# Optimization experiments

Measured on AMD Instinct MI355X. Metric: run time of the kernel, lower is better.

## Reference

```python
import jax, jax.numpy as jnp
import numpy as np

B, NSEQ, SEQ_PER = 2, 4, 256
S = NSEQ * SEQ_PER            # total sequence (stocks interleaved along seq dim)
D, H, HD = 1024, 16, 64       # d_model, nhead, head_dim
HD2, HD4 = HD // 2, HD // 4
DFF = 4096
LAMBDA_INIT = 0.2             # lambda_init_fn(0) = 0.8 - 0.6*exp(0)
SCALING = 1.0 / float(np.sqrt(HD2))
EPS_DEF = float(np.finfo(np.float32).eps)   # torch RMSNorm default eps (eps=None)
EPS_ATTN = 1e-5


def _rms(x, w, eps):
    return x * jax.lax.rsqrt(jnp.mean(x * x, axis=-1, keepdims=True) + eps) * w


def _rope(x, fc):
    # x: (B, T, NSEQ, 2H, HD2); fc: (T, HD4, 2) holding (cos, sin)
    xr = x.reshape(x.shape[:-1] + (HD4, 2))
    c = fc[None, :, None, None, :, 0]
    s = fc[None, :, None, None, :, 1]
    x0, x1 = xr[..., 0], xr[..., 1]
    return jnp.stack([x0 * c - x1 * s, x0 * s + x1 * c], axis=-1).reshape(x.shape)


def setup_inputs():
    key = jax.random.key(0)
    ks = jax.random.split(key, 16)
    def w(i, shape, std=0.02):
        return jax.random.normal(ks[i], shape, jnp.float32) * std
    # true RoPE table for seq_per_stock-1 positions
    t = jnp.arange(SEQ_PER - 1, dtype=jnp.float32)[:, None]
    inv = 1.0 / (10000.0 ** (jnp.arange(HD4, dtype=jnp.float32) / HD4))
    ang = t * inv[None, :]
    return {
        "x": jax.random.normal(ks[0], (B, S, D), jnp.float32),
        "freqs_cis": jnp.stack([jnp.cos(ang), jnp.sin(ang)], axis=-1),
        "w_norm1": jnp.ones((D,), jnp.float32),
        "w_norm2": jnp.ones((D,), jnp.float32),
        "Wq": w(1, (H * HD, D)), "bq": jnp.zeros((H * HD,), jnp.float32),
        "Wk": w(2, (H * HD, D)), "bk": jnp.zeros((H * HD,), jnp.float32),
        "Wv": w(3, (H * HD, D)), "bv": jnp.zeros((H * HD,), jnp.float32),
        "Wo": w(4, (D, H * HD)), "bo": jnp.zeros((D,), jnp.float32),
        "lq1": w(5, (HD2,), 0.1), "lk1": w(6, (HD2,), 0.1),
        "lq2": w(7, (HD2,), 0.1), "lk2": w(8, (HD2,), 0.1),
        "w_attn_norm": jnp.ones((HD,), jnp.float32),
        "Wg": w(9, (2 * DFF, D)), "bg": jnp.zeros((2 * DFF,), jnp.float32),
        "Wout": w(10, (D, DFF)), "bout": jnp.zeros((D,), jnp.float32),
    }


def reference(x, freqs_cis, w_norm1, w_norm2, Wq, bq, Wk, bk, Wv, bv, Wo, bo,
              lq1, lk1, lq2, lk2, w_attn_norm, Wg, bg, Wout, bout):
    Bz, Sz, _ = x.shape
    h = _rms(x, w_norm1, EPS_DEF)
    q = (h @ Wq.T + bq).reshape(Bz, SEQ_PER, NSEQ, 2 * H, HD2)
    k = (h @ Wk.T + bk).reshape(Bz, SEQ_PER, NSEQ, 2 * H, HD2)
    v = (h @ Wv.T + bv).reshape(Bz, Sz, H, HD).transpose(0, 2, 1, 3)   # (B,H,S,HD), interleaved order
    # RoPE on all but the first per-stock timestep; same freqs for every stock
    q = jnp.concatenate([q[:, :1], _rope(q[:, 1:], freqs_cis)], axis=1)
    k = jnp.concatenate([k[:, :1], _rope(k[:, 1:], freqs_cis)], axis=1)
    # reorder q/k to stock-major flat sequence (torch permute(0,4,1,2,3)+reshape)
    q = q.transpose(0, 2, 1, 3, 4).reshape(Bz, Sz, 2 * H, HD2).transpose(0, 2, 1, 3)
    k = k.transpose(0, 2, 1, 3, 4).reshape(Bz, Sz, 2 * H, HD2).transpose(0, 2, 1, 3)
    scores = jnp.einsum('bhqd,bhkd->bhqk', q, k) * SCALING              # (B,2H,S,S)
    causal = jnp.triu(jnp.ones((SEQ_PER, SEQ_PER), bool), 1)
    mask = jnp.tile(causal, (NSEQ, NSEQ))   # block-tiled causal, as torch .repeat
    att = jnp.sign(scores) * jax.nn.softmax(
        jnp.where(mask, -1e30, jnp.abs(scores)), axis=-1)
    lam = jnp.exp(jnp.sum(lk1 * lq1)) - jnp.exp(jnp.sum(lk2 * lq2)) + LAMBDA_INIT
    att = att.reshape(Bz, H, 2, Sz, Sz)
    a1, a2 = att[:, :, 0], att[:, :, 1]
    G = jnp.mean(a1, axis=-2, keepdims=True)          # mean over queries, broadcast back
    a = jnp.where(mask, 0.0, a1 - lam * a2 + lam * G)
    ao = jnp.einsum('bhqk,bhkd->bhqd', a, v)          # v kept in interleaved order (faithful to source)
    ao = _rms(ao, w_attn_norm, EPS_ATTN)
    ao = ao.reshape(Bz, Sz, H * HD)  # flat reinterpret (B,H,S,HD)->(B,S,H*HD), matches torch reshape chain
    x = x + ao @ Wo.T + bo
    h2 = _rms(x, w_norm2, EPS_DEF)
    u, vg = jnp.split(h2 @ Wg.T + bg, 2, axis=-1)
    return x + (u * jax.nn.silu(vg)) @ Wout.T + bout
```

## Files before the change

### kernel.cpp

```cpp
#include <hip/hip_runtime.h>

#define LAMBDA_INIT 0.2f
#define SCALING 0.17677669529663687f
#define EPS_DEF 1.1920928955078125e-07f
#define EPS_ATTN 1e-5f

typedef unsigned short us4 __attribute__((ext_vector_type(4)));
typedef unsigned short us8v __attribute__((ext_vector_type(8)));
typedef float f32x4 __attribute__((ext_vector_type(4)));
typedef float f32x2 __attribute__((ext_vector_type(2)));
typedef __bf16 bf16x8 __attribute__((ext_vector_type(8)));

#define MFMA16(a, b, c) __builtin_amdgcn_mfma_f32_16x16x32_bf16((a), (b), (c), 0, 0, 0)

__device__ __forceinline__ float bf2f(unsigned short u) {
    unsigned int x = ((unsigned int)u) << 16;
    return __builtin_bit_cast(float, x);
}
__device__ __forceinline__ unsigned short f2bf(float f) {
    unsigned int x = __builtin_bit_cast(unsigned int, f);
    x += 0x7fffu + ((x >> 16) & 1u);
    return (unsigned short)(x >> 16);
}
__device__ __forceinline__ void split8(f32x4 a, f32x4 b, us8v& hi, us8v& lo) {
#pragma unroll
    for (int u = 0; u < 4; u++) {
        unsigned short h = f2bf(a[u]);
        hi[u] = h; lo[u] = f2bf(a[u] - bf2f(h));
        unsigned short h2 = f2bf(b[u]);
        hi[4 + u] = h2; lo[4 + u] = f2bf(b[u] - bf2f(h2));
    }
}
__device__ __forceinline__ bf16x8 ldb(const unsigned short* p) {
    return __builtin_bit_cast(bf16x8, *(const us8v*)p);
}

__device__ __forceinline__ float wave_sum(float v) {
#pragma unroll
    for (int o = 32; o > 0; o >>= 1) v += __shfl_down(v, o);
    return v;
}
__device__ __forceinline__ float block_sum(float v, float* red4) {
    int wv = threadIdx.x >> 6;
    float w = wave_sum(v);
    __syncthreads();
    if ((threadIdx.x & 63) == 0) red4[wv] = w;
    __syncthreads();
    return red4[0] + red4[1] + red4[2] + red4[3];
}

__global__ __launch_bounds__(256) void prep(float* __restrict__ G, float* __restrict__ lamp,
                                            const float* lq1, const float* lk1,
                                            const float* lq2, const float* lk2) {
    int i = (blockIdx.x * 256 + threadIdx.x) * 4;
    G[i] = 0.f; G[i + 1] = 0.f; G[i + 2] = 0.f; G[i + 3] = 0.f;
    if (blockIdx.x == 0 && threadIdx.x == 0) {
        float a = 0.f, c = 0.f;
        for (int d = 0; d < 32; d++) {
            a += lq1[d] * lk1[d];
            c += lq2[d] * lk2[d];
        }
        *lamp = expf(a) - expf(c) + LAMBDA_INIT;
    }
}

__global__ __launch_bounds__(256) void cvt_bf16(const float* __restrict__ s,
                                                unsigned short* __restrict__ d, int n4) {
    int i = blockIdx.x * 256 + threadIdx.x;
    if (i >= n4) return;
    f32x4 v = ((const f32x4*)s)[i];
    us4 o;
#pragma unroll
    for (int u = 0; u < 4; u++) o[u] = f2bf(v[u]);
    ((us4*)d)[i] = o;
}

template <int OUTBF>
__global__ __launch_bounds__(256) void rms_kernel(const float* __restrict__ x,
                                                  const float* __restrict__ w,
                                                  void* __restrict__ out, float eps) {
    int row = blockIdx.x;
    int tid = threadIdx.x;
    size_t base = (size_t)row * 1024 + tid * 4;
    f32x4 v = *(const f32x4*)(x + base);
    float ss = v[0]*v[0] + v[1]*v[1] + v[2]*v[2] + v[3]*v[3];
    __shared__ float red4[4];
    float tot = block_sum(ss, red4);
    float r = rsqrtf(tot * (1.0f / 1024.f) + eps);
    f32x4 wv = *(const f32x4*)(w + tid * 4);
    if (OUTBF) {
        us4 o;
#pragma unroll
        for (int i = 0; i < 4; i++) o[i] = f2bf(v[i] * r * wv[i]);
        *(us4*)((unsigned short*)out + base) = o;
    } else {
        f32x4 o;
#pragma unroll
        for (int i = 0; i < 4; i++) o[i] = v[i] * r * wv[i];
        *(f32x4*)((float*)out + base) = o;
    }
}

__global__ __launch_bounds__(256) void gemm_qkv_split(const float* __restrict__ A,
        const float* __restrict__ Wq, const float* __restrict__ Wk, const float* __restrict__ Wv,
        const float* __restrict__ bq, const float* __restrict__ bk, const float* __restrict__ bv,
        float* __restrict__ Yq, float* __restrict__ Yk, float* __restrict__ Yv) {
    const int z = blockIdx.z;
    const float* Bt  = (z == 0) ? Wq : (z == 1) ? Wk : Wv;
    const float* bias= (z == 0) ? bq : (z == 1) ? bk : bv;
    float* out       = (z == 0) ? Yq : (z == 1) ? Yk : Yv;
    const int K = 1024, N = 1024;
    __shared__ __align__(16) unsigned short Ah[64][40];
    __shared__ __align__(16) unsigned short Al[64][40];
    __shared__ __align__(16) unsigned short Bh[64][40];
    __shared__ __align__(16) unsigned short Bl[64][40];
    const int t = threadIdx.x;
    const int bm = blockIdx.x, bn = blockIdx.y;
    const int lane = t & 63, w = t >> 6;
    const int wr = w >> 1, wc = w & 1;
    const int l15 = lane & 15, lg = lane >> 4;
    const int sr = t >> 2, sc = (t & 3) * 8;

    const float* Ag = A + (size_t)(bm * 64 + sr) * K + sc;
    const float* Bg = Bt + (size_t)(bn * 64 + sr) * K + sc;

    f32x4 acc[2][2] = {};

    for (int k0 = 0; k0 < K; k0 += 32) {
        us8v ah, al, bh, bl;
        split8(*(const f32x4*)(Ag + k0), *(const f32x4*)(Ag + k0 + 4), ah, al);
        split8(*(const f32x4*)(Bg + k0), *(const f32x4*)(Bg + k0 + 4), bh, bl);
        __syncthreads();
        *(us8v*)&Ah[sr][sc] = ah;
        *(us8v*)&Al[sr][sc] = al;
        *(us8v*)&Bh[sr][sc] = bh;
        *(us8v*)&Bl[sr][sc] = bl;
        __syncthreads();
        bf16x8 afh[2], afl[2], bfh[2], bfl[2];
#pragma unroll
        for (int mi = 0; mi < 2; mi++) {
            afh[mi] = ldb(&Ah[wr * 32 + mi * 16 + l15][lg * 8]);
            afl[mi] = ldb(&Al[wr * 32 + mi * 16 + l15][lg * 8]);
        }
#pragma unroll
        for (int ni = 0; ni < 2; ni++) {
            bfh[ni] = ldb(&Bh[wc * 32 + ni * 16 + l15][lg * 8]);
            bfl[ni] = ldb(&Bl[wc * 32 + ni * 16 + l15][lg * 8]);
        }
#pragma unroll
        for (int mi = 0; mi < 2; mi++)
#pragma unroll
            for (int ni = 0; ni < 2; ni++) {
                acc[mi][ni] = MFMA16(afl[mi], bfh[ni], acc[mi][ni]);
                acc[mi][ni] = MFMA16(afh[mi], bfl[ni], acc[mi][ni]);
                acc[mi][ni] = MFMA16(afh[mi], bfh[ni], acc[mi][ni]);
            }
    }

    const int rbase = bm * 64 + wr * 32 + (lg << 2);
    const int cbase = bn * 64 + wc * 32 + l15;
#pragma unroll
    for (int mi = 0; mi < 2; mi++) {
#pragma unroll
        for (int ni = 0; ni < 2; ni++) {
            int col = cbase + ni * 16;
            float bb = bias[col];
#pragma unroll
            for (int r = 0; r < 4; r++) {
                int row = rbase + mi * 16 + r;
                out[(size_t)row * N + col] = acc[mi][ni][r] + bb;
            }
        }
    }
}

__global__ __launch_bounds__(256) void gemm_mfma_wb(const unsigned short* __restrict__ A,
                                                    const unsigned short* __restrict__ Bt,
                                                    const float* __restrict__ bias,
                                                    const float* __restrict__ res,
                                                    float* __restrict__ out,
                                                    int M, int N, int K) {
    __shared__ __align__(16) unsigned short As[64][72];
    __shared__ __align__(16) unsigned short Bs[64][72];
    const int t = threadIdx.x;
    const int bm = blockIdx.x, bn = blockIdx.y;
    const int lane = t & 63, w = t >> 6;
    const int wr = w >> 1, wc = w & 1;
    const int l15 = lane & 15, lg = lane >> 4;
    const int sr = t >> 2, sc = (t & 3) * 16;

    const unsigned short* Ag = A + (size_t)(bm * 64 + sr) * K + sc;
    const unsigned short* Bg = Bt + (size_t)(bn * 64 + sr) * K + sc;

    f32x4 acc[2][2] = {};

    for (int k0 = 0; k0 < K; k0 += 64) {
        us8v a0 = *(const us8v*)(Ag + k0);
        us8v a1 = *(const us8v*)(Ag + k0 + 8);
        us8v b0 = *(const us8v*)(Bg + k0);
        us8v b1 = *(const us8v*)(Bg + k0 + 8);
        __syncthreads();
        *(us8v*)&As[sr][sc]     = a0;
        *(us8v*)&As[sr][sc + 8] = a1;
        *(us8v*)&Bs[sr][sc]     = b0;
        *(us8v*)&Bs[sr][sc + 8] = b1;
        __syncthreads();
#pragma unroll
        for (int kk = 0; kk < 2; kk++) {
            bf16x8 af[2], bf[2];
#pragma unroll
            for (int mi = 0; mi < 2; mi++)
                af[mi] = ldb(&As[wr * 32 + mi * 16 + l15][kk * 32 + lg * 8]);
#pragma unroll
            for (int ni = 0; ni < 2; ni++)
                bf[ni] = ldb(&Bs[wc * 32 + ni * 16 + l15][kk * 32 + lg * 8]);
#pragma unroll
            for (int mi = 0; mi < 2; mi++)
#pragma unroll
                for (int ni = 0; ni < 2; ni++)
                    acc[mi][ni] = MFMA16(af[mi], bf[ni], acc[mi][ni]);
        }
    }

    const int rbase = bm * 64 + wr * 32 + (lg << 2);
    const int cbase = bn * 64 + wc * 32 + l15;
#pragma unroll
    for (int mi = 0; mi < 2; mi++) {
#pragma unroll
        for (int ni = 0; ni < 2; ni++) {
            int col = cbase + ni * 16;
            float bb = bias[col];
#pragma unroll
            for (int r = 0; r < 4; r++) {
                int row = rbase + mi * 16 + r;
                size_t oi = (size_t)row * N + col;
                out[oi] = acc[mi][ni][r] + bb + res[oi];
            }
        }
    }
}

__global__ __launch_bounds__(256) void gemm_gate_mfma(const unsigned short* __restrict__ A,
                                                      const float* __restrict__ Wg,
                                                      const float* __restrict__ bg,
                                                      unsigned short* __restrict__ mlp) {
    __shared__ __align__(16) unsigned short As[128][72];
    __shared__ __align__(16) unsigned short BsU[64][72];
    __shared__ __align__(16) unsigned short BsV[64][72];
    const int t = threadIdx.x;
    const int bm = blockIdx.x, bn = blockIdx.y;
    const int lane = t & 63, w = t >> 6;
    const int wr = w >> 1, wc = w & 1;
    const int l15 = lane & 15, lg = lane >> 4;
    const int sr = t >> 2, sc = (t & 3) * 16;

    const unsigned short* Ag  = A + (size_t)(bm * 128 + sr) * 1024 + sc;
    const unsigned short* Ag2 = Ag + (size_t)64 * 1024;
    const float* BgU = Wg + (size_t)(bn * 64 + sr) * 1024 + sc;
    const float* BgV = Wg + (size_t)(4096 + bn * 64 + sr) * 1024 + sc;

    f32x4 accU[4][2] = {};
    f32x4 accV[4][2] = {};

    for (int k0 = 0; k0 < 1024; k0 += 64) {
        us8v a0 = *(const us8v*)(Ag + k0);
        us8v a1 = *(const us8v*)(Ag + k0 + 8);
        us8v a2 = *(const us8v*)(Ag2 + k0);
        us8v a3 = *(const us8v*)(Ag2 + k0 + 8);
        f32x4 u0 = *(const f32x4*)(BgU + k0);
        f32x4 u1 = *(const f32x4*)(BgU + k0 + 4);
        f32x4 u2 = *(const f32x4*)(BgU + k0 + 8);
        f32x4 u3 = *(const f32x4*)(BgU + k0 + 12);
        f32x4 v0 = *(const f32x4*)(BgV + k0);
        f32x4 v1 = *(const f32x4*)(BgV + k0 + 4);
        f32x4 v2 = *(const f32x4*)(BgV + k0 + 8);
        f32x4 v3 = *(const f32x4*)(BgV + k0 + 12);
        us8v uw0, uw1, vw0, vw1;
#pragma unroll
        for (int u = 0; u < 4; u++) {
            uw0[u] = f2bf(u0[u]); uw0[4 + u] = f2bf(u1[u]);
            uw1[u] = f2bf(u2[u]); uw1[4 + u] = f2bf(u3[u]);
            vw0[u] = f2bf(v0[u]); vw0[4 + u] = f2bf(v1[u]);
            vw1[u] = f2bf(v2[u]); vw1[4 + u] = f2bf(v3[u]);
        }
        __syncthreads();
        *(us8v*)&As[sr][sc]          = a0;
        *(us8v*)&As[sr][sc + 8]      = a1;
        *(us8v*)&As[sr + 64][sc]     = a2;
        *(us8v*)&As[sr + 64][sc + 8] = a3;
        *(us8v*)&BsU[sr][sc]         = uw0;
        *(us8v*)&BsU[sr][sc + 8]     = uw1;
        *(us8v*)&BsV[sr][sc]         = vw0;
        *(us8v*)&BsV[sr][sc + 8]     = vw1;
        __syncthreads();
#pragma unroll
        for (int kk = 0; kk < 2; kk++) {
            bf16x8 af[4], bu[2], bv2[2];
#pragma unroll
            for (int mi = 0; mi < 4; mi++)
                af[mi] = ldb(&As[wr * 64 + mi * 16 + l15][kk * 32 + lg * 8]);
#pragma unroll
            for (int ni = 0; ni < 2; ni++) {
                bu[ni]  = ldb(&BsU[wc * 32 + ni * 16 + l15][kk * 32 + lg * 8]);
                bv2[ni] = ldb(&BsV[wc * 32 + ni * 16 + l15][kk * 32 + lg * 8]);
            }
#pragma unroll
            for (int mi = 0; mi < 4; mi++)
#pragma unroll
                for (int ni = 0; ni < 2; ni++) {
                    accU[mi][ni] = MFMA16(af[mi], bu[ni], accU[mi][ni]);
                    accV[mi][ni] = MFMA16(af[mi], bv2[ni], accV[mi][ni]);
                }
        }
    }

    const int rbase = bm * 128 + wr * 64 + (lg << 2);
    const int cbase = bn * 64 + wc * 32 + l15;
#pragma unroll
    for (int mi = 0; mi < 4; mi++) {
#pragma unroll
        for (int ni = 0; ni < 2; ni++) {
            int col = cbase + ni * 16;
            float bu_ = bg[col], bv_ = bg[4096 + col];
#pragma unroll
            for (int r = 0; r < 4; r++) {
                int row = rbase + mi * 16 + r;
                float u = accU[mi][ni][r] + bu_;
                float v = accV[mi][ni][r] + bv_;
                float s = v / (1.f + __expf(-v));
                mlp[(size_t)row * 4096 + col] = f2bf(u * s);
            }
        }
    }
}

__global__ __launch_bounds__(256) void rope_inplace(float* __restrict__ Y,
                                                    const float* __restrict__ fc) {
    int t = blockIdx.x;
    int s = t & 1023;
    int p = s >> 2;
    if (p == 0) return;
    int c0 = threadIdx.x * 4;
    float* y = Y + (size_t)t * 1024 + c0;
    int d4 = (c0 & 31) >> 1;
    f32x4 f = *(const f32x4*)(fc + ((size_t)(p - 1) * 16 + d4) * 2);
    float v0 = y[0], v1 = y[1], v2 = y[2], v3 = y[3];
    y[0] = v0 * f[0] - v1 * f[1];
    y[1] = v0 * f[1] + v1 * f[0];
    y[2] = v2 * f[2] - v3 * f[3];
    y[3] = v2 * f[3] + v3 * f[2];
}

__global__ __launch_bounds__(256) void rope_split_k(const float* __restrict__ Yk,
                                                    const float* __restrict__ fc,
                                                    unsigned short* __restrict__ KhG,
                                                    unsigned short* __restrict__ KlG) {
    int t = blockIdx.x;
    int s = t & 1023;
    int p = s >> 2;
    int c0 = threadIdx.x * 4;
    const float* y = Yk + (size_t)t * 1024 + c0;
    float v0 = y[0], v1 = y[1], v2 = y[2], v3 = y[3];
    if (p > 0) {
        int d4 = (c0 & 31) >> 1;
        f32x4 f = *(const f32x4*)(fc + ((size_t)(p - 1) * 16 + d4) * 2);
        float w0 = v0 * f[0] - v1 * f[1];
        float w1 = v0 * f[1] + v1 * f[0];
        float w2 = v2 * f[2] - v3 * f[3];
        float w3 = v2 * f[3] + v3 * f[2];
        v0 = w0; v1 = w1; v2 = w2; v3 = w3;
    }
    us4 hi, lo;
    hi[0] = f2bf(v0); lo[0] = f2bf(v0 - bf2f(hi[0]));
    hi[1] = f2bf(v1); lo[1] = f2bf(v1 - bf2f(hi[1]));
    hi[2] = f2bf(v2); lo[2] = f2bf(v2 - bf2f(hi[2]));
    hi[3] = f2bf(v3); lo[3] = f2bf(v3 - bf2f(hi[3]));
    *(us4*)(KhG + (size_t)t * 1024 + c0) = hi;
    *(us4*)(KlG + (size_t)t * 1024 + c0) = lo;
}

__global__ __launch_bounds__(256) void v_split_t(const float* __restrict__ Yv,
                                                 unsigned short* __restrict__ VtH,
                                                 unsigned short* __restrict__ VtL) {
    const int jc = blockIdx.x, h = blockIdx.y, b = blockIdx.z;
    __shared__ float tile[64][65];
    const int t = threadIdx.x;
    {
        const int jr = t >> 2, dc = (t & 3) * 16;
        const float* src = Yv + ((size_t)(b * 1024 + jc * 64 + jr) << 10) + h * 64 + dc;
        *(f32x4*)&tile[jr][dc]      = *(const f32x4*)src;
        *(f32x4*)&tile[jr][dc + 4]  = *(const f32x4*)(src + 4);
        *(f32x4*)&tile[jr][dc + 8]  = *(const f32x4*)(src + 8);
        *(f32x4*)&tile[jr][dc + 12] = *(const f32x4*)(src + 12);
    }
    __syncthreads();
    const int d = t >> 2, js = (t & 3) * 16;
    us8v h0, h1, l0, l1;
#pragma unroll
    for (int n = 0; n < 16; n++) {
        float val = tile[js + n][d];
        unsigned short hh = f2bf(val);
        unsigned short ll = f2bf(val - bf2f(hh));
        if (n < 8) { h0[n] = hh; l0[n] = ll; }
        else       { h1[n - 8] = hh; l1[n - 8] = ll; }
    }
    size_t ob = (((size_t)(b * 16 + h) * 64 + d) << 10) + jc * 64 + js;
    *(us8v*)(VtH + ob) = h0; *(us8v*)(VtH + ob + 8) = h1;
    *(us8v*)(VtL + ob) = l0; *(us8v*)(VtL + ob + 8) = l1;
}

__global__ __launch_bounds__(256) void pass_1(const float* __restrict__ Yq,
                                              const unsigned short* __restrict__ KhG,
                                              const unsigned short* __restrict__ KlG,
                                              const unsigned short* __restrict__ VtH,
                                              const unsigned short* __restrict__ VtL,
                                              const float* __restrict__ lamp,
                                              float* __restrict__ G,
                                              float* __restrict__ AOp) {
    const int blk = blockIdx.x;
    const int qc = 15 - (blk >> 5);
    const int h  = blk & 15;
    const int b  = (blk >> 4) & 1;
    const int t = threadIdx.x;
    const int lane = t & 63, w = t >> 6;
    const int l15 = lane & 15, lg = lane >> 4;

    __shared__ __align__(16) unsigned short Kh[64][72];
    __shared__ __align__(16) unsigned short Kl[64][72];
    __shared__ __align__(16) unsigned short Vth[64][72];
    __shared__ __align__(16) unsigned short Vtl[64][72];
    __shared__ __align__(16) unsigned short Wh[64][72];
    __shared__ __align__(16) unsigned short Wl[64][72];
    __shared__ float Gacc[1024];

    for (int i = t; i < 1024; i += 256) Gacc[i] = 0.f;

    us8v qh[2], ql[2];
    {
        const float* qp = Yq + ((size_t)(b * 1024 + qc * 64 + w * 16 + l15) << 10)
                          + h * 64 + lg * 8;
#pragma unroll
        for (int H = 0; H < 2; H++)
            split8(*(const f32x4*)(qp + H * 32), *(const f32x4*)(qp + H * 32 + 4), qh[H], ql[H]);
    }
    const int dq0 = w * 16 + (lg << 2);

    const int srow = t >> 2, ssub = t & 3;
    const int ptk = 4 * (srow & 15) + (srow >> 4);
    const unsigned short* KhB = KhG + ((size_t)(b * 1024) << 10) + h * 64;
    const unsigned short* KlB = KlG + ((size_t)(b * 1024) << 10) + h * 64;
    const unsigned short* VhB = VtH + (((size_t)(b * 16 + h) * 64 + srow) << 10) + ssub * 256;
    const unsigned short* VlB = VtL + (((size_t)(b * 16 + h) * 64 + srow) << 10) + ssub * 256;

    float z1r[4] = {0.f, 0.f, 0.f, 0.f};
    float z2r[4] = {0.f, 0.f, 0.f, 0.f};

    for (int kc = 0; kc <= qc; kc++) {
        __syncthreads();
        {
            const unsigned short* kh = KhB + ((size_t)(kc * 64 + ptk) << 10) + ssub * 16;
            const unsigned short* kl = KlB + ((size_t)(kc * 64 + ptk) << 10) + ssub * 16;
            *(us8v*)&Kh[srow][ssub * 16]     = *(const us8v*)kh;
            *(us8v*)&Kh[srow][ssub * 16 + 8] = *(const us8v*)(kh + 8);
            *(us8v*)&Kl[srow][ssub * 16]     = *(const us8v*)kl;
            *(us8v*)&Kl[srow][ssub * 16 + 8] = *(const us8v*)(kl + 8);
        }
        __syncthreads();
        const int kpos = kc * 16 + l15;
#pragma unroll
        for (int kf = 0; kf < 4; kf++) {
            const int krow = kf * 16 + l15;
            const int kcol = lg * 8;
            bf16x8 b1h = ldb(&Kh[krow][kcol]),      b1l = ldb(&Kl[krow][kcol]);
            bf16x8 b2h = ldb(&Kh[krow][32 + kcol]), b2l = ldb(&Kl[krow][32 + kcol]);
            f32x4 s1 = {}, s2 = {};
            s1 = MFMA16(__builtin_bit_cast(bf16x8, ql[0]), b1h, s1);
            s1 = MFMA16(__builtin_bit_cast(bf16x8, qh[0]), b1l, s1);
            s1 = MFMA16(__builtin_bit_cast(bf16x8, qh[0]), b1h, s1);
            s2 = MFMA16(__builtin_bit_cast(bf16x8, ql[1]), b2h, s2);
            s2 = MFMA16(__builtin_bit_cast(bf16x8, qh[1]), b2l, s2);
            s2 = MFMA16(__builtin_bit_cast(bf16x8, qh[1]), b2h, s2);
#pragma unroll
            for (int r = 0; r < 4; r++) {
                int pq = (qc * 64 + dq0 + r) >> 2;
                if (kpos <= pq) {
                    z1r[r] += __expf(fabsf(s1[r] * SCALING));
                    z2r[r] += __expf(fabsf(s2[r] * SCALING));
                }
            }
        }
    }
#pragma unroll
    for (int r = 0; r < 4; r++) {
        float a = z1r[r];
        a += __shfl_xor(a, 1); a += __shfl_xor(a, 2);
        a += __shfl_xor(a, 4); a += __shfl_xor(a, 8);
        z1r[r] = 1.f / fmaxf(a, 1e-20f);
        float c = z2r[r];
        c += __shfl_xor(c, 1); c += __shfl_xor(c, 2);
        c += __shfl_xor(c, 4); c += __shfl_xor(c, 8);
        z2r[r] = 1.f / fmaxf(c, 1e-20f);
    }
    const float lam = *lamp;

    f32x4 ao[4] = {};

    for (int kc = 0; kc <= qc; kc++) {
        __syncthreads();
        {
            const unsigned short* kh = KhB + ((size_t)(kc * 64 + ptk) << 10) + ssub * 16;
            const unsigned short* kl = KlB + ((size_t)(kc * 64 + ptk) << 10) + ssub * 16;
            *(us8v*)&Kh[srow][ssub * 16]     = *(const us8v*)kh;
            *(us8v*)&Kh[srow][ssub * 16 + 8] = *(const us8v*)(kh + 8);
            *(us8v*)&Kl[srow][ssub * 16]     = *(const us8v*)kl;
            *(us8v*)&Kl[srow][ssub * 16 + 8] = *(const us8v*)(kl + 8);
            const unsigned short* vh = VhB + kc * 16;
            const unsigned short* vl = VlB + kc * 16;
            *(us8v*)&Vth[srow][ssub * 16]     = *(const us8v*)vh;
            *(us8v*)&Vth[srow][ssub * 16 + 8] = *(const us8v*)(vh + 8);
            *(us8v*)&Vtl[srow][ssub * 16]     = *(const us8v*)vl;
            *(us8v*)&Vtl[srow][ssub * 16 + 8] = *(const us8v*)(vl + 8);
        }
        __syncthreads();
        const int kpos = kc * 16 + l15;
#pragma unroll
        for (int kf = 0; kf < 4; kf++) {
            const int krow = kf * 16 + l15;
            const int kcol = lg * 8;
            bf16x8 b1h = ldb(&Kh[krow][kcol]),      b1l = ldb(&Kl[krow][kcol]);
            bf16x8 b2h = ldb(&Kh[krow][32 + kcol]), b2l = ldb(&Kl[krow][32 + kcol]);
            f32x4 s1 = {}, s2 = {};
            s1 = MFMA16(__builtin_bit_cast(bf16x8, ql[0]), b1h, s1);
            s1 = MFMA16(__builtin_bit_cast(bf16x8, qh[0]), b1l, s1);
            s1 = MFMA16(__builtin_bit_cast(bf16x8, qh[0]), b1h, s1);
            s2 = MFMA16(__builtin_bit_cast(bf16x8, ql[1]), b2h, s2);
            s2 = MFMA16(__builtin_bit_cast(bf16x8, qh[1]), b2l, s2);
            s2 = MFMA16(__builtin_bit_cast(bf16x8, qh[1]), b2h, s2);
            const int kli = kf * 16 + l15;
            float colsum = 0.f;
#pragma unroll
            for (int r = 0; r < 4; r++) {
                int pq = (qc * 64 + dq0 + r) >> 2;
                float wv = 0.f, a1 = 0.f;
                if (kpos <= pq) {
                    float t1 = s1[r] * SCALING, t2 = s2[r] * SCALING;
                    float sg1 = (t1 > 0.f) ? 1.f : ((t1 < 0.f) ? -1.f : 0.f);
                    float sg2 = (t2 > 0.f) ? 1.f : ((t2 < 0.f) ? -1.f : 0.f);
                    a1 = sg1 * __expf(fabsf(t1)) * z1r[r];
                    wv = a1 - lam * (sg2 * __expf(fabsf(t2)) * z2r[r]);
                }
                colsum += a1;
                unsigned short hh = f2bf(wv);
                Wh[dq0 + r][kli] = hh;
                Wl[dq0 + r][kli] = f2bf(wv - bf2f(hh));
            }
            colsum += __shfl_xor(colsum, 16);
            colsum += __shfl_xor(colsum, 32);
            if (lane < 16) atomicAdd(&Gacc[kf * 256 + kc * 16 + lane], colsum);
        }
        __syncthreads();
#pragma unroll
        for (int kh2 = 0; kh2 < 2; kh2++) {
            bf16x8 wah = ldb(&Wh[w * 16 + l15][kh2 * 32 + lg * 8]);
            bf16x8 wal = ldb(&Wl[w * 16 + l15][kh2 * 32 + lg * 8]);
#pragma unroll
            for (int df = 0; df < 4; df++) {
                bf16x8 vbh = ldb(&Vth[df * 16 + l15][kh2 * 32 + lg * 8]);
                bf16x8 vbl = ldb(&Vtl[df * 16 + l15][kh2 * 32 + lg * 8]);
                ao[df] = MFMA16(wah, vbl, ao[df]);
                ao[df] = MFMA16(wal, vbh, ao[df]);
                ao[df] = MFMA16(wah, vbh, ao[df]);
            }
        }
    }

#pragma unroll
    for (int df = 0; df < 4; df++) {
#pragma unroll
        for (int r = 0; r < 4; r++) {
            int tq = qc * 64 + dq0 + r;
            int qrow = ((tq & 3) << 8) + (tq >> 2);
            AOp[((((size_t)(b * 16 + h)) << 10) + qrow) * 64 + df * 16 + l15] = ao[df][r];
        }
    }

    __syncthreads();
    float* Gb = G + ((size_t)(b * 16 + h) << 10);
    const int limp = (qc + 1) << 4;
    for (int idx = t; idx < 1024; idx += 256) {
        if ((idx & 255) < limp) atomicAdd(&Gb[idx], Gacc[idx]);
    }
}

__global__ __launch_bounds__(256) void pass_2a(const float* __restrict__ G,
                                               const float* __restrict__ Yv,
                                               float* __restrict__ GVpre) {
    const int h = blockIdx.x, b = blockIdx.y;
    const int t = threadIdx.x;
    __shared__ float Gl[1024];
    __shared__ float S[256][64];
    __shared__ float segsum[4][64];
    for (int i = t; i < 1024; i += 256) Gl[i] = G[((size_t)(b * 16 + h) << 10) + i];
    __syncthreads();
    const int d = t & 63, pg = t >> 6;
    const float* Yvb = Yv + ((size_t)b << 20) + h * 64 + d;
    for (int p0 = 0; p0 < 64; p0++) {
        int pos = pg * 64 + p0;
        float s = 0.f;
#pragma unroll
        for (int sq = 0; sq < 4; sq++) {
            int j = (sq << 8) + pos;
            s += Gl[j] * Yvb[(size_t)j << 10];
        }
        S[pos][d] = s;
    }
    __syncthreads();
    float acc = 0.f;
    for (int p0 = 0; p0 < 64; p0++) {
        int pos = pg * 64 + p0;
        acc += S[pos][d];
        S[pos][d] = acc;
    }
    segsum[pg][d] = acc;
    __syncthreads();
    float off = 0.f;
    for (int g = 0; g < pg; g++) off += segsum[g][d];
    float* gv = GVpre + (((size_t)(b * 16 + h)) << 14) + d;
    for (int p0 = 0; p0 < 64; p0++) {
        int pos = pg * 64 + p0;
        gv[pos << 6] = S[pos][d] + off;
    }
}

__global__ __launch_bounds__(256) void pass_2b(const float* __restrict__ AOp,
                                               const float* __restrict__ GVpre,
                                               const float* __restrict__ lamp,
                                               const float* __restrict__ wan,
                                               unsigned short* __restrict__ aoS) {
    const int qg = blockIdx.x;
    const int h = blockIdx.y, b = blockIdx.z;
    const int t = threadIdx.x;
    const int d = t & 63, rg = t >> 6;
    const float lamg = (*lamp) * (1.f / 1024.f);
    const float wv = wan[d];
    const float* aob = AOp + ((((size_t)(b * 16 + h)) << 10) + (qg << 8)) * 64 + d;
    const float* gvb = GVpre + (((size_t)(b * 16 + h)) << 14) + d;
    unsigned short* ob = aoS + ((size_t)b << 20) + ((size_t)h << 16) + ((size_t)(qg << 8) << 6) + d;
    for (int p0 = 0; p0 < 64; p0++) {
        int pq = p0 * 4 + rg;
        float ao = aob[(size_t)pq << 6] + lamg * gvb[(size_t)pq << 6];
        float ss = ao * ao;
#pragma unroll
        for (int o = 1; o < 64; o <<= 1) ss += __shfl_xor(ss, o);
        float rr_ = rsqrtf(ss * (1.f / 64.f) + EPS_ATTN);
        ob[(size_t)pq << 6] = f2bf(ao * rr_ * wv);
    }
}

extern "C" void kernel_launch(void* const* d_in, const int* in_sizes, int n_in,
                              void* d_out, int out_size, void* d_ws, size_t ws_size,
                              hipStream_t stream) {
    const float* x    = (const float*)d_in[0];
    const float* fc   = (const float*)d_in[1];
    const float* w1   = (const float*)d_in[2];
    const float* w2   = (const float*)d_in[3];
    const float* Wq   = (const float*)d_in[4];
    const float* bq   = (const float*)d_in[5];
    const float* Wk   = (const float*)d_in[6];
    const float* bk   = (const float*)d_in[7];
    const float* Wv   = (const float*)d_in[8];
    const float* bv   = (const float*)d_in[9];
    const float* Wo   = (const float*)d_in[10];
    const float* bo   = (const float*)d_in[11];
    const float* lq1  = (const float*)d_in[12];
    const float* lk1  = (const float*)d_in[13];
    const float* lq2  = (const float*)d_in[14];
    const float* lk2  = (const float*)d_in[15];
    const float* wan  = (const float*)d_in[16];
    const float* Wg   = (const float*)d_in[17];
    const float* bg   = (const float*)d_in[18];
    const float* Wout = (const float*)d_in[19];
    const float* bout = (const float*)d_in[20];

    char* ws = (char*)d_ws;
    const size_t MB = 1024 * 1024;
    float* G    = (float*)(ws);
    float* lam  = (float*)(ws + 256 * 1024);
    float* h32  = (float*)(ws + 1 * MB);
    float* Yq   = (float*)(ws + 9 * MB);
    float* Yk   = (float*)(ws + 17 * MB);
    float* Yv   = (float*)(ws + 25 * MB);
    float* AOp  = (float*)(ws + 33 * MB);
    float* GVpre= (float*)(ws + 41 * MB);
    unsigned short* WoB   = (unsigned short*)(ws + 43 * MB);
    unsigned short* WoutB = (unsigned short*)(ws + 45 * MB);
    unsigned short* KhG = (unsigned short*)(ws + 1 * MB);
    unsigned short* KlG = (unsigned short*)(ws + 5 * MB);
    unsigned short* VtH = (unsigned short*)(ws + 17 * MB);
    unsigned short* VtL = (unsigned short*)(ws + 21 * MB);
    unsigned short* aoS = (unsigned short*)(ws + 1 * MB);
    float* X1           = (float*)(ws + 9 * MB);
    unsigned short* h2b = (unsigned short*)(ws + 5 * MB);
    unsigned short* mlp = (unsigned short*)(ws + 17 * MB);

    prep<<<32, 256, 0, stream>>>(G, lam, lq1, lk1, lq2, lk2);
    cvt_bf16<<<1024, 256, 0, stream>>>(Wo, WoB, 262144);
    cvt_bf16<<<4096, 256, 0, stream>>>(Wout, WoutB, 1048576);
    rms_kernel<0><<<2048, 256, 0, stream>>>(x, w1, h32, EPS_DEF);
    gemm_qkv_split<<<dim3(32, 16, 3), 256, 0, stream>>>(h32, Wq, Wk, Wv, bq, bk, bv, Yq, Yk, Yv);
    rope_inplace<<<2048, 256, 0, stream>>>(Yq, fc);
    rope_split_k<<<2048, 256, 0, stream>>>(Yk, fc, KhG, KlG);
    v_split_t<<<dim3(16, 16, 2), 256, 0, stream>>>(Yv, VtH, VtL);
    pass_1<<<512, 256, 0, stream>>>(Yq, KhG, KlG, VtH, VtL, lam, G, AOp);
    pass_2a<<<dim3(16, 2), 256, 0, stream>>>(G, Yv, GVpre);
    pass_2b<<<dim3(4, 16, 2), 256, 0, stream>>>(AOp, GVpre, lam, wan, aoS);
    dim3 gmf(32, 16);
    gemm_mfma_wb<<<gmf, 256, 0, stream>>>(aoS, WoB, bo, x, X1, 2048, 1024, 1024);
    rms_kernel<1><<<2048, 256, 0, stream>>>(X1, w2, h2b, EPS_DEF);
    gemm_gate_mfma<<<dim3(16, 64), 256, 0, stream>>>(h2b, Wg, bg, mlp);
    gemm_mfma_wb<<<gmf, 256, 0, stream>>>(mlp, WoutB, bout, X1, (float*)d_out, 2048, 1024, 4096);
}
```

Baseline: 476.2 us.

## Pre-split QKV operands to bf16 hi/lo and pair causal query chunks per block

The QKV GEMM now reads operands that were already split into bf16 hi/lo planes by separate kernels (rms_split, cvt_split for the weights). It uses a 64-wide K step, which removes the per-tile fp32 split work and halves the number of loop iterations and barriers. pass_1 now launches 256 blocks, each handling query chunk 15-p and then chunk p, so every block does the same amount of causal work. The trade-offs are extra weight-conversion launches and traffic, bigger shared tiles, and lower grid parallelism in the attention pass.

Result: faster. 464.4 us (-2.5%).

```diff
diff --git a/kernel.cpp b/kernel.cpp
--- a/kernel.cpp
+++ b/kernel.cpp
@@ -73,6 +73,22 @@
 #pragma unroll
     for (int u = 0; u < 4; u++) o[u] = f2bf(v[u]);
     ((us4*)d)[i] = o;
+}
+
+__global__ __launch_bounds__(256) void cvt_split(const float* __restrict__ s,
+                                                 unsigned short* __restrict__ hi,
+                                                 unsigned short* __restrict__ lo, int n4) {
+    int i = blockIdx.x * 256 + threadIdx.x;
+    if (i >= n4) return;
+    f32x4 v = ((const f32x4*)s)[i];
+    us4 h, l;
+#pragma unroll
+    for (int u = 0; u < 4; u++) {
+        h[u] = f2bf(v[u]);
+        l[u] = f2bf(v[u] - bf2f(h[u]));
+    }
+    ((us4*)hi)[i] = h;
+    ((us4*)lo)[i] = l;
 }
 
 template <int OUTBF>
@@ -101,60 +117,94 @@
     }
 }
 
-__global__ __launch_bounds__(256) void gemm_qkv_split(const float* __restrict__ A,
-        const float* __restrict__ Wq, const float* __restrict__ Wk, const float* __restrict__ Wv,
+__global__ __launch_bounds__(256) void rms_split(const float* __restrict__ x,
+                                                 const float* __restrict__ w,
+                                                 unsigned short* __restrict__ hh,
+                                                 unsigned short* __restrict__ hl, float eps) {
+    int row = blockIdx.x;
+    int tid = threadIdx.x;
+    size_t base = (size_t)row * 1024 + tid * 4;
+    f32x4 v = *(const f32x4*)(x + base);
+    float ss = v[0]*v[0] + v[1]*v[1] + v[2]*v[2] + v[3]*v[3];
+    __shared__ float red4[4];
+    float tot = block_sum(ss, red4);
+    float r = rsqrtf(tot * (1.0f / 1024.f) + eps);
+    f32x4 wv = *(const f32x4*)(w + tid * 4);
+    us4 oh, ol;
+#pragma unroll
+    for (int i = 0; i < 4; i++) {
+        float val = v[i] * r * wv[i];
+        oh[i] = f2bf(val);
+        ol[i] = f2bf(val - bf2f(oh[i]));
+    }
+    *(us4*)(hh + base) = oh;
+    *(us4*)(hl + base) = ol;
+}
+
+__global__ __launch_bounds__(256) void gemm_qkv_ps(
+        const unsigned short* __restrict__ AH, const unsigned short* __restrict__ AL,
+        const unsigned short* __restrict__ WqH, const unsigned short* __restrict__ WqL,
+        const unsigned short* __restrict__ WkH, const unsigned short* __restrict__ WkL,
+        const unsigned short* __restrict__ WvH, const unsigned short* __restrict__ WvL,
         const float* __restrict__ bq, const float* __restrict__ bk, const float* __restrict__ bv,
         float* __restrict__ Yq, float* __restrict__ Yk, float* __restrict__ Yv) {
     const int z = blockIdx.z;
-    const float* Bt  = (z == 0) ? Wq : (z == 1) ? Wk : Wv;
-    const float* bias= (z == 0) ? bq : (z == 1) ? bk : bv;
-    float* out       = (z == 0) ? Yq : (z == 1) ? Yk : Yv;
+    const unsigned short* BH = (z == 0) ? WqH : (z == 1) ? WkH : WvH;
+    const unsigned short* BL = (z == 0) ? WqL : (z == 1) ? WkL : WvL;
+    const float* bias = (z == 0) ? bq : (z == 1) ? bk : bv;
+    float* out        = (z == 0) ? Yq : (z == 1) ? Yk : Yv;
     const int K = 1024, N = 1024;
-    __shared__ __align__(16) unsigned short Ah[64][40];
-    __shared__ __align__(16) unsigned short Al[64][40];
-    __shared__ __align__(16) unsigned short Bh[64][40];
-    __shared__ __align__(16) unsigned short Bl[64][40];
+    __shared__ __align__(16) unsigned short Ah[64][72];
+    __shared__ __align__(16) unsigned short Al[64][72];
+    __shared__ __align__(16) unsigned short Bh[64][72];
+    __shared__ __align__(16) unsigned short Bl[64][72];
     const int t = threadIdx.x;
     const int bm = blockIdx.x, bn = blockIdx.y;
     const int lane = t & 63, w = t >> 6;
     const int wr = w >> 1, wc = w & 1;
     const int l15 = lane & 15, lg = lane >> 4;
-    const int sr = t >> 2, sc = (t & 3) * 8;
-
-    const float* Ag = A + (size_t)(bm * 64 + sr) * K + sc;
-    const float* Bg = Bt + (size_t)(bn * 64 + sr) * K + sc;
+    const int sr = t >> 2, sc = (t & 3) * 16;
+
+    const unsigned short* AgH = AH + (size_t)(bm * 64 + sr) * K + sc;
+    const unsigned short* AgL = AL + (size_t)(bm * 64 + sr) * K + sc;
+    const unsigned short* BgH = BH + (size_t)(bn * 64 + sr) * K + sc;
+    const unsigned short* BgL = BL + (size_t)(bn * 64 + sr) * K + sc;
 
     f32x4 acc[2][2] = {};
 
-    for (int k0 = 0; k0 < K; k0 += 32) {
-        us8v ah, al, bh, bl;
-        split8(*(const f32x4*)(Ag + k0), *(const f32x4*)(Ag + k0 + 4), ah, al);
-        split8(*(const f32x4*)(Bg + k0), *(const f32x4*)(Bg + k0 + 4), bh, bl);
+    for (int k0 = 0; k0 < K; k0 += 64) {
+        us8v ah0 = *(const us8v*)(AgH + k0), ah1 = *(const us8v*)(AgH + k0 + 8);
+        us8v al0 = *(const us8v*)(AgL + k0), al1 = *(const us8v*)(AgL + k0 + 8);
+        us8v bh0 = *(const us8v*)(BgH + k0), bh1 = *(const us8v*)(BgH + k0 + 8);
+        us8v bl0 = *(const us8v*)(BgL + k0), bl1 = *(const us8v*)(BgL + k0 + 8);
         __syncthreads();
-        *(us8v*)&Ah[sr][sc] = ah;
-        *(us8v*)&Al[sr][sc] = al;
-        *(us8v*)&Bh[sr][sc] = bh;
-        *(us8v*)&Bl[sr][sc] = bl;
+        *(us8v*)&Ah[sr][sc] = ah0; *(us8v*)&Ah[sr][sc + 8] = ah1;
+        *(us8v*)&Al[sr][sc] = al0; *(us8v*)&Al[sr][sc + 8] = al1;
+        *(us8v*)&Bh[sr][sc] = bh0; *(us8v*)&Bh[sr][sc + 8] = bh1;
+        *(us8v*)&Bl[sr][sc] = bl0; *(us8v*)&Bl[sr][sc + 8] = bl1;
         __syncthreads();
-        bf16x8 afh[2], afl[2], bfh[2], bfl[2];
-#pragma unroll
-        for (int mi = 0; mi < 2; mi++) {
-            afh[mi] = ldb(&Ah[wr * 32 + mi * 16 + l15][lg * 8]);
-            afl[mi] = ldb(&Al[wr * 32 + mi * 16 + l15][lg * 8]);
-        }
-#pragma unroll
-        for (int ni = 0; ni < 2; ni++) {
-            bfh[ni] = ldb(&Bh[wc * 32 + ni * 16 + l15][lg * 8]);
-            bfl[ni] = ldb(&Bl[wc * 32 + ni * 16 + l15][lg * 8]);
-        }
-#pragma unroll
-        for (int mi = 0; mi < 2; mi++)
+#pragma unroll
+        for (int kk = 0; kk < 2; kk++) {
+            bf16x8 afh[2], afl[2], bfh[2], bfl[2];
+#pragma unroll
+            for (int mi = 0; mi < 2; mi++) {
+                afh[mi] = ldb(&Ah[wr * 32 + mi * 16 + l15][kk * 32 + lg * 8]);
+                afl[mi] = ldb(&Al[wr * 32 + mi * 16 + l15][kk * 32 + lg * 8]);
+            }
 #pragma unroll
             for (int ni = 0; ni < 2; ni++) {
-                acc[mi][ni] = MFMA16(afl[mi], bfh[ni], acc[mi][ni]);
-                acc[mi][ni] = MFMA16(afh[mi], bfl[ni], acc[mi][ni]);
-                acc[mi][ni] = MFMA16(afh[mi], bfh[ni], acc[mi][ni]);
-            }
+                bfh[ni] = ldb(&Bh[wc * 32 + ni * 16 + l15][kk * 32 + lg * 8]);
+                bfl[ni] = ldb(&Bl[wc * 32 + ni * 16 + l15][kk * 32 + lg * 8]);
+            }
+#pragma unroll
+            for (int mi = 0; mi < 2; mi++)
+#pragma unroll
+                for (int ni = 0; ni < 2; ni++) {
+                    acc[mi][ni] = MFMA16(afl[mi], bfh[ni], acc[mi][ni]);
+                    acc[mi][ni] = MFMA16(afh[mi], bfl[ni], acc[mi][ni]);
+                    acc[mi][ni] = MFMA16(afh[mi], bfh[ni], acc[mi][ni]);
+                }
+        }
     }
 
     const int rbase = bm * 64 + wr * 32 + (lg << 2);
@@ -418,7 +468,7 @@
                                               float* __restrict__ G,
                                               float* __restrict__ AOp) {
     const int blk = blockIdx.x;
-    const int qc = 15 - (blk >> 5);
+    const int p  = blk >> 5;
     const int h  = blk & 15;
     const int b  = (blk >> 4) & 1;
     const int t = threadIdx.x;
@@ -435,158 +485,162 @@
 
     for (int i = t; i < 1024; i += 256) Gacc[i] = 0.f;
 
-    us8v qh[2], ql[2];
-    {
-        const float* qp = Yq + ((size_t)(b * 1024 + qc * 64 + w * 16 + l15) << 10)
-                          + h * 64 + lg * 8;
-#pragma unroll
-        for (int H = 0; H < 2; H++)
-            split8(*(const f32x4*)(qp + H * 32), *(const f32x4*)(qp + H * 32 + 4), qh[H], ql[H]);
-    }
-    const int dq0 = w * 16 + (lg << 2);
-
     const int srow = t >> 2, ssub = t & 3;
     const int ptk = 4 * (srow & 15) + (srow >> 4);
     const unsigned short* KhB = KhG + ((size_t)(b * 1024) << 10) + h * 64;
     const unsigned short* KlB = KlG + ((size_t)(b * 1024) << 10) + h * 64;
     const unsigned short* VhB = VtH + (((size_t)(b * 16 + h) * 64 + srow) << 10) + ssub * 256;
     const unsigned short* VlB = VtL + (((size_t)(b * 16 + h) * 64 + srow) << 10) + ssub * 256;
-
-    float z1r[4] = {0.f, 0.f, 0.f, 0.f};
-    float z2r[4] = {0.f, 0.f, 0.f, 0.f};
-
-    for (int kc = 0; kc <= qc; kc++) {
-        __syncthreads();
+    const float lam = *lamp;
+    const int dq0 = w * 16 + (lg << 2);
+
+    for (int qq = 0; qq < 2; qq++) {
+        const int qc = qq ? p : (15 - p);
+
+        us8v qh[2], ql[2];
         {
-            const unsigned short* kh = KhB + ((size_t)(kc * 64 + ptk) << 10) + ssub * 16;
-            const unsigned short* kl = KlB + ((size_t)(kc * 64 + ptk) << 10) + ssub * 16;
-            *(us8v*)&Kh[srow][ssub * 16]     = *(const us8v*)kh;
-            *(us8v*)&Kh[srow][ssub * 16 + 8] = *(const us8v*)(kh + 8);
-            *(us8v*)&Kl[srow][ssub * 16]     = *(const us8v*)kl;
-            *(us8v*)&Kl[srow][ssub * 16 + 8] = *(const us8v*)(kl + 8);
-        }
-        __syncthreads();
-        const int kpos = kc * 16 + l15;
-#pragma unroll
-        for (int kf = 0; kf < 4; kf++) {
-            const int krow = kf * 16 + l15;
-            const int kcol = lg * 8;
-            bf16x8 b1h = ldb(&Kh[krow][kcol]),      b1l = ldb(&Kl[krow][kcol]);
-            bf16x8 b2h = ldb(&Kh[krow][32 + kcol]), b2l = ldb(&Kl[krow][32 + kcol]);
-            f32x4 s1 = {}, s2 = {};
-            s1 = MFMA16(__builtin_bit_cast(bf16x8, ql[0]), b1h, s1);
-            s1 = MFMA16(__builtin_bit_cast(bf16x8, qh[0]), b1l, s1);
-            s1 = MFMA16(__builtin_bit_cast(bf16x8, qh[0]), b1h, s1);
-            s2 = MFMA16(__builtin_bit_cast(bf16x8, ql[1]), b2h, s2);
-            s2 = MFMA16(__builtin_bit_cast(bf16x8, qh[1]), b2l, s2);
-            s2 = MFMA16(__builtin_bit_cast(bf16x8, qh[1]), b2h, s2);
+            const float* qp = Yq + ((size_t)(b * 1024 + qc * 64 + w * 16 + l15) << 10)
+                              + h * 64 + lg * 8;
+#pragma unroll
+            for (int H = 0; H < 2; H++)
+                split8(*(const f32x4*)(qp + H * 32), *(const f32x4*)(qp + H * 32 + 4), qh[H], ql[H]);
+        }
+
+        float z1r[4] = {0.f, 0.f, 0.f, 0.f};
+        float z2r[4] = {0.f, 0.f, 0.f, 0.f};
+
+        for (int kc = 0; kc <= qc; kc++) {
+            __syncthreads();
+            {
+                const unsigned short* kh = KhB + ((size_t)(kc * 64 + ptk) << 10) + ssub * 16;
+                const unsigned short* kl = KlB + ((size_t)(kc * 64 + ptk) << 10) + ssub * 16;
+                *(us8v*)&Kh[srow][ssub * 16]     = *(const us8v*)kh;
+                *(us8v*)&Kh[srow][ssub * 16 + 8] = *(const us8v*)(kh + 8);
+                *(us8v*)&Kl[srow][ssub * 16]     = *(const us8v*)kl;
+                *(us8v*)&Kl[srow][ssub * 16 + 8] = *(const us8v*)(kl + 8);
+            }
+            __syncthreads();
+            const int kpos = kc * 16 + l15;
+#pragma unroll
+            for (int kf = 0; kf < 4; kf++) {
+                const int krow = kf * 16 + l15;
+                const int kcol = lg * 8;
+                bf16x8 b1h = ldb(&Kh[krow][kcol]),      b1l = ldb(&Kl[krow][kcol]);
+                bf16x8 b2h = ldb(&Kh[krow][32 + kcol]), b2l = ldb(&Kl[krow][32 + kcol]);
+                f32x4 s1 = {}, s2 = {};
+                s1 = MFMA16(__builtin_bit_cast(bf16x8, ql[0]), b1h, s1);
+                s1 = MFMA16(__builtin_bit_cast(bf16x8, qh[0]), b1l, s1);
+                s1 = MFMA16(__builtin_bit_cast(bf16x8, qh[0]), b1h, s1);
+                s2 = MFMA16(__builtin_bit_cast(bf16x8, ql[1]), b2h, s2);
+                s2 = MFMA16(__builtin_bit_cast(bf16x8, qh[1]), b2l, s2);
+                s2 = MFMA16(__builtin_bit_cast(bf16x8, qh[1]), b2h, s2);
+#pragma unroll
+                for (int r = 0; r < 4; r++) {
+                    int pq = (qc * 64 + dq0 + r) >> 2;
+                    if (kpos <= pq) {
+                        z1r[r] += __expf(fabsf(s1[r] * SCALING));
+                        z2r[r] += __expf(fabsf(s2[r] * SCALING));
+                    }
+                }
+            }
+        }
+#pragma unroll
+        for (int r = 0; r < 4; r++) {
+            float a = z1r[r];
+            a += __shfl_xor(a, 1); a += __shfl_xor(a, 2);
+            a += __shfl_xor(a, 4); a += __shfl_xor(a, 8);
+            z1r[r] = 1.f / fmaxf(a, 1e-20f);
+            float c = z2r[r];
+            c += __shfl_xor(c, 1); c += __shfl_xor(c, 2);
+            c += __shfl_xor(c, 4); c += __shfl_xor(c, 8);
+            z2r[r] = 1.f / fmaxf(c, 1e-20f);
+        }
+
+        f32x4 ao[4] = {};
+
+        for (int kc = 0; kc <= qc; kc++) {
+            __syncthreads();
+            {
+                const unsigned short* kh = KhB + ((size_t)(kc * 64 + ptk) << 10) + ssub * 16;
+                const unsigned short* kl = KlB + ((size_t)(kc * 64 + ptk) << 10) + ssub * 16;
+                *(us8v*)&Kh[srow][ssub * 16]     = *(const us8v*)kh;
+                *(us8v*)&Kh[srow][ssub * 16 + 8] = *(const us8v*)(kh + 8);
+                *(us8v*)&Kl[srow][ssub * 16]     = *(const us8v*)kl;
+                *(us8v*)&Kl[srow][ssub * 16 + 8] = *(const us8v*)(kl + 8);
+                const unsigned short* vh = VhB + kc * 16;
+                const unsigned short* vl = VlB + kc * 16;
+                *(us8v*)&Vth[srow][ssub * 16]     = *(const us8v*)vh;
+                *(us8v*)&Vth[srow][ssub * 16 + 8] = *(const us8v*)(vh + 8);
+                *(us8v*)&Vtl[srow][ssub * 16]     = *(const us8v*)vl;
+                *(us8v*)&Vtl[srow][ssub * 16 + 8] = *(const us8v*)(vl + 8);
+            }
+            __syncthreads();
+            const int kpos = kc * 16 + l15;
+#pragma unroll
+            for (int kf = 0; kf < 4; kf++) {
+                const int krow = kf * 16 + l15;
+                const int kcol = lg * 8;
+                bf16x8 b1h = ldb(&Kh[krow][kcol]),      b1l = ldb(&Kl[krow][kcol]);
+                bf16x8 b2h = ldb(&Kh[krow][32 + kcol]), b2l = ldb(&Kl[krow][32 + kcol]);
+                f32x4 s1 = {}, s2 = {};
+                s1 = MFMA16(__builtin_bit_cast(bf16x8, ql[0]), b1h, s1);
+                s1 = MFMA16(__builtin_bit_cast(bf16x8, qh[0]), b1l, s1);
+                s1 = MFMA16(__builtin_bit_cast(bf16x8, qh[0]), b1h, s1);
+                s2 = MFMA16(__builtin_bit_cast(bf16x8, ql[1]), b2h, s2);
+                s2 = MFMA16(__builtin_bit_cast(bf16x8, qh[1]), b2l, s2);
+                s2 = MFMA16(__builtin_bit_cast(bf16x8, qh[1]), b2h, s2);
+                const int kli = kf * 16 + l15;
+                float colsum = 0.f;
+#pragma unroll
+                for (int r = 0; r < 4; r++) {
+                    int pq = (qc * 64 + dq0 + r) >> 2;
+                    float wv = 0.f, a1 = 0.f;
+                    if (kpos <= pq) {
+                        float t1 = s1[r] * SCALING, t2 = s2[r] * SCALING;
+                        float sg1 = (t1 > 0.f) ? 1.f : ((t1 < 0.f) ? -1.f : 0.f);
+                        float sg2 = (t2 > 0.f) ? 1.f : ((t2 < 0.f) ? -1.f : 0.f);
+                        a1 = sg1 * __expf(fabsf(t1)) * z1r[r];
+                        wv = a1 - lam * (sg2 * __expf(fabsf(t2)) * z2r[r]);
+                    }
+                    colsum += a1;
+                    unsigned short hh = f2bf(wv);
+                    Wh[dq0 + r][kli] = hh;
+                    Wl[dq0 + r][kli] = f2bf(wv - bf2f(hh));
+                }
+                colsum += __shfl_xor(colsum, 16);
+                colsum += __shfl_xor(colsum, 32);
+                if (lane < 16) atomicAdd(&Gacc[kf * 256 + kc * 16 + lane], colsum);
+            }
+            __syncthreads();
+#pragma unroll
+            for (int kh2 = 0; kh2 < 2; kh2++) {
+                bf16x8 wah = ldb(&Wh[w * 16 + l15][kh2 * 32 + lg * 8]);
+                bf16x8 wal = ldb(&Wl[w * 16 + l15][kh2 * 32 + lg * 8]);
+#pragma unroll
+                for (int df = 0; df < 4; df++) {
+                    bf16x8 vbh = ldb(&Vth[df * 16 + l15][kh2 * 32 + lg * 8]);
+                    bf16x8 vbl = ldb(&Vtl[df * 16 + l15][kh2 * 32 + lg * 8]);
+                    ao[df] = MFMA16(wah, vbl, ao[df]);
+                    ao[df] = MFMA16(wal, vbh, ao[df]);
+                    ao[df] = MFMA16(wah, vbh, ao[df]);
+                }
+            }
+        }
+
+#pragma unroll
+        for (int df = 0; df < 4; df++) {
 #pragma unroll
             for (int r = 0; r < 4; r++) {
-                int pq = (qc * 64 + dq0 + r) >> 2;
-                if (kpos <= pq) {
-                    z1r[r] += __expf(fabsf(s1[r] * SCALING));
-                    z2r[r] += __expf(fabsf(s2[r] * SCALING));
-                }
-            }
-        }
-    }
-#pragma unroll
-    for (int r = 0; r < 4; r++) {
-        float a = z1r[r];
-        a += __shfl_xor(a, 1); a += __shfl_xor(a, 2);
-        a += __shfl_xor(a, 4); a += __shfl_xor(a, 8);
-        z1r[r] = 1.f / fmaxf(a, 1e-20f);
-        float c = z2r[r];
-        c += __shfl_xor(c, 1); c += __shfl_xor(c, 2);
-        c += __shfl_xor(c, 4); c += __shfl_xor(c, 8);
-        z2r[r] = 1.f / fmaxf(c, 1e-20f);
-    }
-    const float lam = *lamp;
-
-    f32x4 ao[4] = {};
-
-    for (int kc = 0; kc <= qc; kc++) {
-        __syncthreads();
-        {
-            const unsigned short* kh = KhB + ((size_t)(kc * 64 + ptk) << 10) + ssub * 16;
-            const unsigned short* kl = KlB + ((size_t)(kc * 64 + ptk) << 10) + ssub * 16;
-            *(us8v*)&Kh[srow][ssub * 16]     = *(const us8v*)kh;
-            *(us8v*)&Kh[srow][ssub * 16 + 8] = *(const us8v*)(kh + 8);
-            *(us8v*)&Kl[srow][ssub * 16]     = *(const us8v*)kl;
-            *(us8v*)&Kl[srow][ssub * 16 + 8] = *(const us8v*)(kl + 8);
-            const unsigned short* vh = VhB + kc * 16;
-            const unsigned short* vl = VlB + kc * 16;
-            *(us8v*)&Vth[srow][ssub * 16]     = *(const us8v*)vh;
-            *(us8v*)&Vth[srow][ssub * 16 + 8] = *(const us8v*)(vh + 8);
-            *(us8v*)&Vtl[srow][ssub * 16]     = *(const us8v*)vl;
-            *(us8v*)&Vtl[srow][ssub * 16 + 8] = *(const us8v*)(vl + 8);
-        }
-        __syncthreads();
-        const int kpos = kc * 16 + l15;
-#pragma unroll
-        for (int kf = 0; kf < 4; kf++) {
-            const int krow = kf * 16 + l15;
-            const int kcol = lg * 8;
-            bf16x8 b1h = ldb(&Kh[krow][kcol]),      b1l = ldb(&Kl[krow][kcol]);
-            bf16x8 b2h = ldb(&Kh[krow][32 + kcol]), b2l = ldb(&Kl[krow][32 + kcol]);
-            f32x4 s1 = {}, s2 = {};
-            s1 = MFMA16(__builtin_bit_cast(bf16x8, ql[0]), b1h, s1);
-            s1 = MFMA16(__builtin_bit_cast(bf16x8, qh[0]), b1l, s1);
-            s1 = MFMA16(__builtin_bit_cast(bf16x8, qh[0]), b1h, s1);
-            s2 = MFMA16(__builtin_bit_cast(bf16x8, ql[1]), b2h, s2);
-            s2 = MFMA16(__builtin_bit_cast(bf16x8, qh[1]), b2l, s2);
-            s2 = MFMA16(__builtin_bit_cast(bf16x8, qh[1]), b2h, s2);
-            const int kli = kf * 16 + l15;
-            float colsum = 0.f;
-#pragma unroll
-            for (int r = 0; r < 4; r++) {
-                int pq = (qc * 64 + dq0 + r) >> 2;
-                float wv = 0.f, a1 = 0.f;
-                if (kpos <= pq) {
-                    float t1 = s1[r] * SCALING, t2 = s2[r] * SCALING;
-                    float sg1 = (t1 > 0.f) ? 1.f : ((t1 < 0.f) ? -1.f : 0.f);
-                    float sg2 = (t2 > 0.f) ? 1.f : ((t2 < 0.f) ? -1.f : 0.f);
-                    a1 = sg1 * __expf(fabsf(t1)) * z1r[r];
-                    wv = a1 - lam * (sg2 * __expf(fabsf(t2)) * z2r[r]);
-                }
-                colsum += a1;
-                unsigned short hh = f2bf(wv);
-                Wh[dq0 + r][kli] = hh;
-                Wl[dq0 + r][kli] = f2bf(wv - bf2f(hh));
-            }
-            colsum += __shfl_xor(colsum, 16);
-            colsum += __shfl_xor(colsum, 32);
-            if (lane < 16) atomicAdd(&Gacc[kf * 256 + kc * 16 + lane], colsum);
-        }
-        __syncthreads();
-#pragma unroll
-        for (int kh2 = 0; kh2 < 2; kh2++) {
-            bf16x8 wah = ldb(&Wh[w * 16 + l15][kh2 * 32 + lg * 8]);
-            bf16x8 wal = ldb(&Wl[w * 16 + l15][kh2 * 32 + lg * 8]);
-#pragma unroll
-            for (int df = 0; df < 4; df++) {
-                bf16x8 vbh = ldb(&Vth[df * 16 + l15][kh2 * 32 + lg * 8]);
-                bf16x8 vbl = ldb(&Vtl[df * 16 + l15][kh2 * 32 + lg * 8]);
-                ao[df] = MFMA16(wah, vbl, ao[df]);
-                ao[df] = MFMA16(wal, vbh, ao[df]);
-                ao[df] = MFMA16(wah, vbh, ao[df]);
-            }
-        }
-    }
-
-#pragma unroll
-    for (int df = 0; df < 4; df++) {
-#pragma unroll
-        for (int r = 0; r < 4; r++) {
-            int tq = qc * 64 + dq0 + r;
-            int qrow = ((tq & 3) << 8) + (tq >> 2);
-            AOp[((((size_t)(b * 16 + h)) << 10) + qrow) * 64 + df * 16 + l15] = ao[df][r];
+                int tq = qc * 64 + dq0 + r;
+                int qrow = ((tq & 3) << 8) + (tq >> 2);
+                AOp[((((size_t)(b * 16 + h)) << 10) + qrow) * 64 + df * 16 + l15] = ao[df][r];
+            }
         }
     }
 
     __syncthreads();
     float* Gb = G + ((size_t)(b * 16 + h) << 10);
-    const int limp = (qc + 1) << 4;
+    const int limp = (16 - p) << 4;
     for (int idx = t; idx < 1024; idx += 256) {
         if ((idx & 255) < limp) atomicAdd(&Gb[idx], Gacc[idx]);
     }
@@ -686,14 +740,21 @@
     const size_t MB = 1024 * 1024;
     float* G    = (float*)(ws);
     float* lam  = (float*)(ws + 256 * 1024);
-    float* h32  = (float*)(ws + 1 * MB);
+    unsigned short* hH = (unsigned short*)(ws + 1 * MB);
+    unsigned short* hL = (unsigned short*)(ws + 5 * MB);
     float* Yq   = (float*)(ws + 9 * MB);
     float* Yk   = (float*)(ws + 17 * MB);
     float* Yv   = (float*)(ws + 25 * MB);
+    unsigned short* WqH = (unsigned short*)(ws + 33 * MB);
+    unsigned short* WqL = (unsigned short*)(ws + 35 * MB);
+    unsigned short* WkH = (unsigned short*)(ws + 37 * MB);
+    unsigned short* WkL = (unsigned short*)(ws + 39 * MB);
+    unsigned short* WvH = (unsigned short*)(ws + 41 * MB);
+    unsigned short* WvL = (unsigned short*)(ws + 43 * MB);
+    unsigned short* WoutB = (unsigned short*)(ws + 45 * MB);
     float* AOp  = (float*)(ws + 33 * MB);
     float* GVpre= (float*)(ws + 41 * MB);
-    unsigned short* WoB   = (unsigned short*)(ws + 43 * MB);
-    unsigned short* WoutB = (unsigned short*)(ws + 45 * MB);
+    unsigned short* WoB = (unsigned short*)(ws + 43 * MB);
     unsigned short* KhG = (unsigned short*)(ws + 1 * MB);
     unsigned short* KlG = (unsigned short*)(ws + 5 * MB);
     unsigned short* VtH = (unsigned short*)(ws + 17 * MB);
@@ -704,14 +765,18 @@
     unsigned short* mlp = (unsigned short*)(ws + 17 * MB);
 
     prep<<<32, 256, 0, stream>>>(G, lam, lq1, lk1, lq2, lk2);
+    cvt_bf16<<<4096, 256, 0, stream>>>(Wout, WoutB, 1048576);
+    rms_split<<<2048, 256, 0, stream>>>(x, w1, hH, hL, EPS_DEF);
+    cvt_split<<<1024, 256, 0, stream>>>(Wq, WqH, WqL, 262144);
+    cvt_split<<<1024, 256, 0, stream>>>(Wk, WkH, WkL, 262144);
+    cvt_split<<<1024, 256, 0, stream>>>(Wv, WvH, WvL, 262144);
+    gemm_qkv_ps<<<dim3(32, 16, 3), 256, 0, stream>>>(hH, hL, WqH, WqL, WkH, WkL, WvH, WvL,
+                                                     bq, bk, bv, Yq, Yk, Yv);
     cvt_bf16<<<1024, 256, 0, stream>>>(Wo, WoB, 262144);
-    cvt_bf16<<<4096, 256, 0, stream>>>(Wout, WoutB, 1048576);
-    rms_kernel<0><<<2048, 256, 0, stream>>>(x, w1, h32, EPS_DEF);
-    gemm_qkv_split<<<dim3(32, 16, 3), 256, 0, stream>>>(h32, Wq, Wk, Wv, bq, bk, bv, Yq, Yk, Yv);
     rope_inplace<<<2048, 256, 0, stream>>>(Yq, fc);
     rope_split_k<<<2048, 256, 0, stream>>>(Yk, fc, KhG, KlG);
     v_split_t<<<dim3(16, 16, 2), 256, 0, stream>>>(Yv, VtH, VtL);
-    pass_1<<<512, 256, 0, stream>>>(Yq, KhG, KlG, VtH, VtL, lam, G, AOp);
+    pass_1<<<256, 256, 0, stream>>>(Yq, KhG, KlG, VtH, VtL, lam, G, AOp);
     pass_2a<<<dim3(16, 2), 256, 0, stream>>>(G, Yv, GVpre);
     pass_2b<<<dim3(4, 16, 2), 256, 0, stream>>>(AOp, GVpre, lam, wan, aoS);
     dim3 gmf(32, 16);
```
